# Kernel optimization log

Hardware: AMD Instinct MI355X
Metric: run time of the kernel (lower is better)

The kernel has to match this reference:

```python
import jax, jax.numpy as jnp
import numpy as np

N = 50000      # nodes
E = 800000     # edges
H = 128        # hidden_features
DEPTH = 5
G = 64         # graphs in batch
EPS = 1e-5


def _ln(x, g, b):
    m = jnp.mean(x, axis=-1, keepdims=True)
    v = jnp.mean((x - m) ** 2, axis=-1, keepdims=True)
    return (x - m) * jax.lax.rsqrt(v + EPS) * g + b


def _lin_init(key, fan_in, fan_out):
    s = 1.0 / np.sqrt(fan_in)
    kw, kb = jax.random.split(key)
    return (jax.random.uniform(kw, (fan_in, fan_out), jnp.float32, -s, s),
            jax.random.uniform(kb, (fan_out,), jnp.float32, -s, s))


def setup_inputs() -> dict:
    key = jax.random.key(0)
    ks = jax.random.split(key, 16)
    inp = {
        'x': jax.random.normal(ks[0], (N, 1), jnp.float32),
        'pos': jax.random.normal(ks[1], (N, 3), jnp.float32),
        'edge_index': jax.random.randint(ks[2], (2, E), 0, N, jnp.int32),
        'cell_offset': jax.random.normal(ks[3], (E, 3), jnp.float32),
        'unit_cell': jax.random.normal(ks[4], (3, 3), jnp.float32),
        'batch_ids': jnp.sort(jax.random.randint(ks[5], (N,), 0, G, jnp.int32)),
    }
    inp['emb_w'], inp['emb_b'] = _lin_init(ks[6], 1, H)
    # stacked per-layer params for lax.scan
    def stack(fn):
        outs = [fn(jax.random.fold_in(ks[7], i)) for i in range(DEPTH)]
        return tuple(jnp.stack(t) for t in zip(*outs))
    def layer_params(k):
        k1, k2, k3, k4 = jax.random.split(k, 4)
        mw1, mb1 = _lin_init(k1, 2 * H + 1, H)
        mw2, mb2 = _lin_init(k2, H, H)
        uw1, ub1 = _lin_init(k3, 2 * H, H)
        uw2, ub2 = _lin_init(k4, H, H)
        ones = jnp.ones((H,), jnp.float32); zeros = jnp.zeros((H,), jnp.float32)
        return (mw1, mb1, ones, zeros, mw2, mb2, ones, zeros,
                uw1, ub1, ones, zeros, uw2, ub2, ones, zeros)
    (inp['msg_w1'], inp['msg_b1'], inp['msg_g1'], inp['msg_be1'],
     inp['msg_w2'], inp['msg_b2'], inp['msg_g2'], inp['msg_be2'],
     inp['upd_w1'], inp['upd_b1'], inp['upd_g1'], inp['upd_be1'],
     inp['upd_w2'], inp['upd_b2'], inp['upd_g2'], inp['upd_be2']) = stack(layer_params)
    inp['pred_w1'], inp['pred_b1'] = _lin_init(ks[8], H, H)
    inp['pred_w2'], inp['pred_b2'] = _lin_init(ks[9], H, 1)
    return inp


def reference(x, pos, edge_index, cell_offset, unit_cell, batch_ids,
              emb_w, emb_b,
              msg_w1, msg_b1, msg_g1, msg_be1, msg_w2, msg_b2, msg_g2, msg_be2,
              upd_w1, upd_b1, upd_g1, upd_be1, upd_w2, upd_b2, upd_g2, upd_be2,
              pred_w1, pred_b1, pred_w2, pred_b2):
    src, dst = edge_index[0], edge_index[1]  # PyG: x_j = source, x_i = target
    h = x @ emb_w + emb_b  # [N, H]
    # PBC distances
    corrected = pos[dst] - cell_offset @ unit_cell  # [E, 3]
    dist = jnp.linalg.norm(corrected - pos[src], axis=-1, keepdims=True)  # [E, 1]

    def step(h, p):
        (mw1, mb1, mg1, mbe1, mw2, mb2, mg2, mbe2,
         uw1, ub1, ug1, ube1, uw2, ub2, ug2, ube2) = p
        msg = jnp.concatenate([h[dst], h[src], dist], axis=-1)  # [E, 2H+1]
        msg = jax.nn.relu(_ln(msg @ mw1 + mb1, mg1, mbe1))
        msg = jax.nn.relu(_ln(msg @ mw2 + mb2, mg2, mbe2))
        aggr = jax.ops.segment_sum(msg, dst, num_segments=N)  # scatter-add to targets
        u = jnp.concatenate([h, aggr], axis=-1)  # [N, 2H]
        u = jax.nn.relu(_ln(u @ uw1 + ub1, ug1, ube1))
        u = jax.nn.relu(_ln(u @ uw2 + ub2, ug2, ube2))
        return h + u, None  # residual

    params = (msg_w1, msg_b1, msg_g1, msg_be1, msg_w2, msg_b2, msg_g2, msg_be2,
              upd_w1, upd_b1, upd_g1, upd_be1, upd_w2, upd_b2, upd_g2, upd_be2)
    h, _ = jax.lax.scan(step, h, params)
    pooled = jax.ops.segment_sum(h, batch_ids, num_segments=G)  # global_add_pool
    return jax.nn.relu(pooled @ pred_w1 + pred_b1) @ pred_w2 + pred_b2  # [G, 1]
```

## Files before the change

kernel.cpp:

```cpp
#include <hip/hip_runtime.h>
#include <hip/hip_bf16.h>

#define NN 50000
#define NE 800000
#define HD 128
#define DEPTH 5
#define NG 64
#define LNEPS 1e-5f

typedef __attribute__((ext_vector_type(8))) short bf8;
typedef __attribute__((ext_vector_type(4))) float f4;

static __device__ __forceinline__ unsigned short bf1(float x) {
    __hip_bfloat16 b = __float2bfloat16(x);
    unsigned short r;
    __builtin_memcpy(&r, &b, 2);
    return r;
}
static __device__ __forceinline__ unsigned int cvt2(float a, float b) {
    float2 t; t.x = a; t.y = b;
    __hip_bfloat162 h = __float22bfloat162_rn(t);
    unsigned int r;
    __builtin_memcpy(&r, &h, 4);
    return r;
}


__global__ void pack_weights(const float* __restrict__ msg_w1, const float* __restrict__ msg_w2,
                             const float* __restrict__ upd_w1, const float* __restrict__ upd_w2,
                             unsigned short* __restrict__ packed) {
    const int which = blockIdx.y & 3, layer = blockIdx.y >> 2;
    const int t = blockIdx.x * 256 + threadIdx.x;
    unsigned short* lbase = packed + layer * 98304;
    if (which == 0) {
        if (t >= 32768) return;
        const int e = t & 7, l = (t >> 3) & 63, f = (t >> 9) & 15, s = t >> 13;
        const int kk = s*32 + ((l >> 4) << 3) + e;
        const int k = (kk & 7)*16 + (kk >> 3);
        const float* W = msg_w1 + layer*257*HD;
        const float v = (f < 8) ? W[k*HD + f*16 + (l & 15)]
                                : W[(k + 128)*HD + (f - 8)*16 + (l & 15)];
        lbase[t] = bf1(v);
        return;
    }
    const float* src; int K; unsigned short* dst;
    if (which == 1)      { src = msg_w2 + layer*HD*HD;  K = 128; dst = lbase + 32768; }
    else if (which == 2) { src = upd_w1 + layer*256*HD; K = 256; dst = lbase + 49152; }
    else                 { src = upd_w2 + layer*HD*HD;  K = 128; dst = lbase + 81920; }
    if (t >= K * HD) return;
    const int e = t & 7, l = (t >> 3) & 63, f = (t >> 9) & 7, s = t >> 12;
    const int kk = s*32 + ((l >> 4) << 3) + e;
    const int k = (which & 1) ? ((kk & 7)*16 + (kk >> 3)) : kk;
    const int n = f*16 + (l & 15);
    dst[t] = bf1(src[k*HD + n]);
}

__global__ void pack_sig(const float* __restrict__ msg_w1, const float* __restrict__ msg_g1,
                         const float* __restrict__ msg_be1, float* __restrict__ sig) {
    const int t = blockIdx.x * 256 + threadIdx.x;
    if (t >= DEPTH * 384) return;
    const int layer = t / 384, w3 = (t % 384) / 128, i = t % 128;
    const int col = (i & 7)*16 + (i >> 3);
    float v;
    if (w3 == 0)      v = msg_w1[layer*257*HD + 256*HD + col];
    else if (w3 == 1) v = msg_g1[layer*HD + col];
    else              v = msg_be1[layer*HD + col];
    sig[t] = v;
}

__global__ void pack_y0(const float* __restrict__ emb_w, const float* __restrict__ emb_b,
                        const float* __restrict__ msg_w1, const float* __restrict__ msg_b1,
                        float* __restrict__ y0ab) {
    const int t = threadIdx.x;
    const int half = t >> 7, c = t & 127;
    const float* W = msg_w1 + half*128*HD;
    float a = 0.f, b = 0.f;
    for (int k = 0; k < 128; ++k) {
        const float w = W[k*HD + c];
        a += emb_w[k] * w;
        b += emb_b[k] * w;
    }
    if (half == 0) b += msg_b1[c];
    const int i = half*128 + ((c & 15)*8 + (c >> 4));
    y0ab[i] = a; y0ab[256 + i] = b;
}

__global__ void embed_kernel(const float* __restrict__ x, const float* __restrict__ emb_w,
                             const float* __restrict__ emb_b, const float* __restrict__ y0ab,
                             float* __restrict__ h, unsigned short* __restrict__ hb,
                             unsigned short* __restrict__ y) {
    const int i = blockIdx.x * 256 + threadIdx.x;
    const int n = i >> 8, t = i & 255;
    const float xv = x[n];
    y[i] = bf1(xv * y0ab[t] + y0ab[256 + t]);
    if (t < 128) {
        const float v = xv * emb_w[t] + emb_b[t];
        h[n*HD + t] = v; hb[n*HD + t] = bf1(v);
    }
}

__global__ void hist_kernel(const int* __restrict__ ei, int* __restrict__ cnt) {
    const int e = blockIdx.x * 256 + threadIdx.x;
    atomicAdd(&cnt[ei[NE + e]], 1);
}

__global__ __launch_bounds__(1024) void scan_kernel(const int* __restrict__ cnt,
                                                    int* __restrict__ cur) {
    __shared__ int part[1024];
    const int t = threadIdx.x;
    const int per = 49;
    const int base = t * per;
    int s = 0;
    for (int i = 0; i < per; ++i) { const int idx = base + i; if (idx < NN) s += cnt[idx]; }
    part[t] = s; __syncthreads();
    for (int st = 1; st < 1024; st <<= 1) {
        const int v = (t >= st) ? part[t - st] : 0;
        __syncthreads();
        part[t] += v;
        __syncthreads();
    }
    int run = (t == 0) ? 0 : part[t - 1];
    for (int i = 0; i < per; ++i) {
        const int idx = base + i;
        if (idx < NN) { cur[idx] = run; run += cnt[idx]; }
    }
}

__global__ void scatter_kernel(const int* __restrict__ ei, int* __restrict__ cur,
                               int* __restrict__ sidx, int* __restrict__ ssrc,
                               int* __restrict__ sdst) {
    const int e = blockIdx.x * 256 + threadIdx.x;
    const int d = ei[NE + e];
    const int p = atomicAdd(&cur[d], 1);
    sidx[p] = e; ssrc[p] = ei[e]; sdst[p] = d;
}

__global__ void dist_kernel(const float* __restrict__ pos, const int* __restrict__ sidx,
                            const int* __restrict__ ssrc, const int* __restrict__ sdst,
                            const float* __restrict__ cell, const float* __restrict__ U,
                            float* __restrict__ dist) {
    const int p = blockIdx.x * 256 + threadIdx.x;
    const int e = sidx[p];
    const int s = ssrc[p], d = sdst[p];
    const float c0 = cell[e*3], c1 = cell[e*3+1], c2 = cell[e*3+2];
    const float ox = c0*U[0] + c1*U[3] + c2*U[6];
    const float oy = c0*U[1] + c1*U[4] + c2*U[7];
    const float oz = c0*U[2] + c1*U[5] + c2*U[8];
    const float dx = pos[d*3]   - ox - pos[s*3];
    const float dy = pos[d*3+1] - oy - pos[s*3+1];
    const float dz = pos[d*3+2] - oz - pos[s*3+2];
    dist[p] = sqrtf(dx*dx + dy*dy + dz*dz);
}

__global__ __launch_bounds__(128, 4) void edge_kernel(
    const unsigned short* __restrict__ y, const float* __restrict__ dist,
    const int* __restrict__ ssrc, const int* __restrict__ sdst,
    const unsigned short* __restrict__ pw2, const float* __restrict__ sig,
    const float* __restrict__ b2, const float* __restrict__ g2,
    const float* __restrict__ be2, float* __restrict__ aggr)
{
    __shared__ unsigned short lds[64 * 128];
    __shared__ int dstl[64];
    char* ldsb = (char*)lds;
    const int tid = threadIdx.x, blk = blockIdx.x;
    const int l = tid & 63, wv = tid >> 6;
    const int li = l & 15, gq = l >> 4;

    if (tid < 64) dstl[tid] = sdst[blk*64 + tid];

    {
        const int rl = l >> 1, half = l & 1;
        const int row = wv*32 + rl;
        const int e = blk*64 + row;
        const int dn = sdst[e], sn = ssrc[e];
        const float dv = dist[e];
        const unsigned short* pd = y + dn*256 + half*64;
        const unsigned short* pS = y + sn*256 + 128 + half*64;
        const float* wl = sig + half*64;

        float msum[64];
        #pragma unroll
        for (int c = 0; c < 8; ++c) {
            const uint4 ud = *(const uint4*)(pd + c*8);
            const uint4 us = *(const uint4*)(pS + c*8);
            const float4 wa = *(const float4*)(wl + c*8);
            const float4 wb = *(const float4*)(wl + c*8 + 4);
            const unsigned int du[4] = {ud.x, ud.y, ud.z, ud.w};
            const unsigned int su[4] = {us.x, us.y, us.z, us.w};
            const float ww[8] = {wa.x,wa.y,wa.z,wa.w, wb.x,wb.y,wb.z,wb.w};
            #pragma unroll
            for (int k = 0; k < 4; ++k) {
                const float d0 = __uint_as_float(du[k] << 16);
                const float d1 = __uint_as_float(du[k] & 0xffff0000u);
                const float s0 = __uint_as_float(su[k] << 16);
                const float s1 = __uint_as_float(su[k] & 0xffff0000u);
                msum[c*8 + 2*k]     = d0 + s0 + dv*ww[2*k];
                msum[c*8 + 2*k + 1] = d1 + s1 + dv*ww[2*k+1];
            }
        }
        float s1 = 0.f, s2 = 0.f;
        #pragma unroll
        for (int i = 0; i < 64; ++i) { s1 += msum[i]; s2 += msum[i]*msum[i]; }
        s1 += __shfl_xor(s1, 1);
        s2 += __shfl_xor(s2, 1);
        const float mean = s1 * (1.f/HD);
        const float rstd = rsqrtf(s2*(1.f/HD) - mean*mean + LNEPS);

        const float* g1p = sig + 128 + half*64;
        const float* e1p = sig + 256 + half*64;
        const int rsw = (row & 7) << 4;
        const int base = row*256 + half*128;
        #pragma unroll
        for (int c = 0; c < 8; ++c) {
            const float4 ga = *(const float4*)(g1p + c*8);
            const float4 gb = *(const float4*)(g1p + c*8 + 4);
            const float4 ea = *(const float4*)(e1p + c*8);
            const float4 eb = *(const float4*)(e1p + c*8 + 4);
            const float gg[8] = {ga.x,ga.y,ga.z,ga.w, gb.x,gb.y,gb.z,gb.w};
            const float ee[8] = {ea.x,ea.y,ea.z,ea.w, eb.x,eb.y,eb.z,eb.w};
            float t[8];
            #pragma unroll
            for (int k = 0; k < 8; ++k)
                t[k] = fmaxf((msum[c*8+k] - mean)*rstd*gg[k] + ee[k], 0.f);
            uint4 u;
            u.x = cvt2(t[0], t[1]); u.y = cvt2(t[2], t[3]);
            u.z = cvt2(t[4], t[5]); u.w = cvt2(t[6], t[7]);
            *(uint4*)(ldsb + ((base + c*16) ^ rsw)) = u;
        }
    }

    f4 acc2[2][8];
    #pragma unroll
    for (int m = 0; m < 2; ++m)
        #pragma unroll
        for (int f = 0; f < 8; ++f) { f4 z = {0.f,0.f,0.f,0.f}; acc2[m][f] = z; }
    #pragma unroll
    for (int s = 0; s < 4; ++s) {
        bf8 breg[8];
        #pragma unroll
        for (int f = 0; f < 8; ++f) breg[f] = *(const bf8*)(pw2 + s*4096 + f*512 + l*8);
        #pragma unroll
        for (int m = 0; m < 2; ++m) {
            const int ar = wv*32 + m*16 + li;
            const bf8 a = *(const bf8*)(ldsb + ((ar*256 + s*64 + gq*16) ^ ((ar & 7) << 4)));
            #pragma unroll
            for (int f = 0; f < 8; ++f)
                acc2[m][f] = __builtin_amdgcn_mfma_f32_16x16x32_bf16(a, breg[f], acc2[m][f], 0, 0, 0);
        }
    }

    {
        float bb2[8], gg2[8], be2v[8];
        #pragma unroll
        for (int f = 0; f < 8; ++f) {
            const int n = f*16 + li;
            bb2[f] = b2[n]; gg2[f] = g2[n]; be2v[f] = be2[n];
        }
        #pragma unroll
        for (int m = 0; m < 2; ++m) {
            float ps[4] = {0,0,0,0}, pq[4] = {0,0,0,0};
            #pragma unroll
            for (int f = 0; f < 8; ++f)
                #pragma unroll
                for (int r = 0; r < 4; ++r) {
                    const float v = acc2[m][f][r] + bb2[f];
                    acc2[m][f][r] = v;
                    ps[r] += v; pq[r] += v*v;
                }
            #pragma unroll
            for (int mm = 1; mm < 16; mm <<= 1)
                #pragma unroll
                for (int r = 0; r < 4; ++r) {
                    ps[r] += __shfl_xor(ps[r], mm);
                    pq[r] += __shfl_xor(pq[r], mm);
                }
            #pragma unroll
            for (int r = 0; r < 4; ++r) {
                const float mean = ps[r] * (1.f/HD);
                const float rstd = rsqrtf(pq[r]*(1.f/HD) - mean*mean + LNEPS);
                const int row = wv*32 + m*16 + gq*4 + r;
                float vv[8];
                #pragma unroll
                for (int f = 0; f < 8; ++f)
                    vv[f] = fmaxf((acc2[m][f][r] - mean)*rstd*gg2[f] + be2v[f], 0.f);
                uint4 u;
                u.x = cvt2(vv[0], vv[1]); u.y = cvt2(vv[2], vv[3]);
                u.z = cvt2(vv[4], vv[5]); u.w = cvt2(vv[6], vv[7]);
                *(uint4*)(ldsb + ((row*256 + li*16) ^ ((row & 7) << 4))) = u;
            }
        }
    }
    __syncthreads();

    {
        const int j = tid;
        const int jj = (j & 7)*16 + (j >> 3);
        int curd = dstl[0];
        float a0 = 0.f;
        #pragma unroll 4
        for (int row = 0; row < 64; ++row) {
            const int d = dstl[row];
            const unsigned short u = *(const unsigned short*)(ldsb + ((row*256 + j*2) ^ ((row & 7) << 4)));
            const float v = __uint_as_float(((unsigned int)u) << 16);
            if (d != curd) { unsafeAtomicAdd(&aggr[curd*HD + jj], a0); a0 = 0.f; curd = d; }
            a0 += v;
        }
        unsafeAtomicAdd(&aggr[curd*HD + jj], a0);
    }
}

__global__ __launch_bounds__(256, 4) void node_kernel(
    unsigned short* __restrict__ hb, float* __restrict__ aggr,
    const unsigned short* __restrict__ pw,
    const float* __restrict__ b1, const float* __restrict__ g1, const float* __restrict__ be1,
    const float* __restrict__ b2, const float* __restrict__ g2, const float* __restrict__ be2,
    float* __restrict__ h,
    const unsigned short* __restrict__ pwy, const float* __restrict__ b1y,
    unsigned short* __restrict__ y, int do_y)
{
    __shared__ unsigned short lds[64 * 128];
    char* ldsb = (char*)lds;
    const int tid = threadIdx.x, blk = blockIdx.x;
    const int l = tid & 63, wv = tid >> 6;
    const int li = l & 15, gq = l >> 4;

    const int row = wv*16 + li;
    const int nA = blk*64 + row;
    const int nc = (nA < NN) ? nA : NN - 1;
    const unsigned short* pH = hb + nc*HD + gq*8;
    float* pA = aggr + nc*HD + gq*8;

    f4 acc[8];
    #pragma unroll
    for (int f = 0; f < 8; ++f) { f4 z = {0.f,0.f,0.f,0.f}; acc[f] = z; }

    #pragma unroll
    for (int s = 0; s < 8; ++s) {
        bf8 breg[8];
        #pragma unroll
        for (int f = 0; f < 8; ++f) breg[f] = *(const bf8*)(pw + s*4096 + f*512 + l*8);
        bf8 a;
        if (s < 4) {
            a = *(const bf8*)(pH + s*32);
        } else {
            const float4 a0 = *(const float4*)(pA + (s-4)*32);
            const float4 a1 = *(const float4*)(pA + (s-4)*32 + 4);
            union { unsigned int u[4]; bf8 v; } pk;
            pk.u[0] = cvt2(a0.x, a0.y); pk.u[1] = cvt2(a0.z, a0.w);
            pk.u[2] = cvt2(a1.x, a1.y); pk.u[3] = cvt2(a1.z, a1.w);
            a = pk.v;
        }
        #pragma unroll
        for (int f = 0; f < 8; ++f)
            acc[f] = __builtin_amdgcn_mfma_f32_16x16x32_bf16(a, breg[f], acc[f], 0, 0, 0);
    }

    {
        const float4 z = {0.f,0.f,0.f,0.f};
        if (nA < NN) {
            #pragma unroll
            for (int s = 0; s < 4; ++s) { *(float4*)(pA + s*32) = z; *(float4*)(pA + s*32 + 4) = z; }
        }
    }

    {
        float bb[8], gg[8], be[8];
        #pragma unroll
        for (int f = 0; f < 8; ++f) {
            const int n = f*16 + li;
            bb[f] = b1[n]; gg[f] = g1[n]; be[f] = be1[n];
        }
        float ps[4] = {0,0,0,0}, pq[4] = {0,0,0,0};
        #pragma unroll
        for (int f = 0; f < 8; ++f)
            #pragma unroll
            for (int r = 0; r < 4; ++r) {
                const float v = acc[f][r] + bb[f];
                acc[f][r] = v;
                ps[r] += v; pq[r] += v*v;
            }
        #pragma unroll
        for (int mm = 1; mm < 16; mm <<= 1)
            #pragma unroll
            for (int r = 0; r < 4; ++r) {
                ps[r] += __shfl_xor(ps[r], mm);
                pq[r] += __shfl_xor(pq[r], mm);
            }
        #pragma unroll
        for (int r = 0; r < 4; ++r) {
            const float mean = ps[r] * (1.f/HD);
            const float rstd = rsqrtf(pq[r]*(1.f/HD) - mean*mean + LNEPS);
            const int rw = wv*16 + gq*4 + r;
            float vv[8];
            #pragma unroll
            for (int f = 0; f < 8; ++f)
                vv[f] = fmaxf((acc[f][r] - mean)*rstd*gg[f] + be[f], 0.f);
            uint4 u;
            u.x = cvt2(vv[0], vv[1]); u.y = cvt2(vv[2], vv[3]);
            u.z = cvt2(vv[4], vv[5]); u.w = cvt2(vv[6], vv[7]);
            *(uint4*)(ldsb + ((rw*256 + li*16) ^ ((rw & 15) << 4))) = u;
        }
    }

    const unsigned short* pw2 = pw + 32768;
    f4 acc2[8];
    #pragma unroll
    for (int f = 0; f < 8; ++f) { f4 z = {0.f,0.f,0.f,0.f}; acc2[f] = z; }
    #pragma unroll
    for (int s = 0; s < 4; ++s) {
        bf8 breg[8];
        #pragma unroll
        for (int f = 0; f < 8; ++f) breg[f] = *(const bf8*)(pw2 + s*4096 + f*512 + l*8);
        const int ar = wv*16 + li;
        const bf8 a = *(const bf8*)(ldsb + ((ar*256 + s*64 + gq*16) ^ ((ar & 15) << 4)));
        #pragma unroll
        for (int f = 0; f < 8; ++f)
            acc2[f] = __builtin_amdgcn_mfma_f32_16x16x32_bf16(a, breg[f], acc2[f], 0, 0, 0);
    }

    {
        float bb2[8], gg2[8], be2v[8];
        #pragma unroll
        for (int f = 0; f < 8; ++f) {
            const int n = f*16 + li;
            bb2[f] = b2[n]; gg2[f] = g2[n]; be2v[f] = be2[n];
        }
        float ps[4] = {0,0,0,0}, pq[4] = {0,0,0,0};
        #pragma unroll
        for (int f = 0; f < 8; ++f)
            #pragma unroll
            for (int r = 0; r < 4; ++r) {
                const float v = acc2[f][r] + bb2[f];
                acc2[f][r] = v;
                ps[r] += v; pq[r] += v*v;
            }
        #pragma unroll
        for (int mm = 1; mm < 16; mm <<= 1)
            #pragma unroll
            for (int r = 0; r < 4; ++r) {
                ps[r] += __shfl_xor(ps[r], mm);
                pq[r] += __shfl_xor(pq[r], mm);
            }
        #pragma unroll
        for (int r = 0; r < 4; ++r) {
            const int node = blk*64 + wv*16 + gq*4 + r;
            const float mean = ps[r] * (1.f/HD);
            const float rstd = rsqrtf(pq[r]*(1.f/HD) - mean*mean + LNEPS);
            const int rw = wv*16 + gq*4 + r;
            float nhv[8];
            if (node < NN) {
                #pragma unroll
                for (int f = 0; f < 8; ++f) {
                    const int n = f*16 + li;
                    float v = fmaxf((acc2[f][r] - mean)*rstd*gg2[f] + be2v[f], 0.f);
                    const int idx = node*HD + n;
                    const float nh = h[idx] + v;
                    h[idx] = nh; hb[idx] = bf1(nh);
                    nhv[f] = nh;
                }
            } else {
                #pragma unroll
                for (int f = 0; f < 8; ++f) nhv[f] = 0.f;
            }
            uint4 u;
            u.x = cvt2(nhv[0], nhv[1]); u.y = cvt2(nhv[2], nhv[3]);
            u.z = cvt2(nhv[4], nhv[5]); u.w = cvt2(nhv[6], nhv[7]);
            *(uint4*)(ldsb + ((rw*256 + li*16) ^ ((rw & 15) << 4))) = u;
        }
    }

    if (do_y) {
        f4 accy[16];
        #pragma unroll
        for (int f = 0; f < 16; ++f) { f4 z = {0.f,0.f,0.f,0.f}; accy[f] = z; }
        #pragma unroll
        for (int s = 0; s < 4; ++s) {
            const int ar = wv*16 + li;
            const bf8 a = *(const bf8*)(ldsb + ((ar*256 + s*64 + gq*16) ^ ((ar & 15) << 4)));
            #pragma unroll
            for (int fh = 0; fh < 2; ++fh) {
                bf8 breg[8];
                #pragma unroll
                for (int f = 0; f < 8; ++f)
                    breg[f] = *(const bf8*)(pwy + s*8192 + (fh*8 + f)*512 + l*8);
                #pragma unroll
                for (int f = 0; f < 8; ++f)
                    accy[fh*8 + f] = __builtin_amdgcn_mfma_f32_16x16x32_bf16(a, breg[f], accy[fh*8 + f], 0, 0, 0);
            }
        }
        float bv[8];
        #pragma unroll
        for (int f = 0; f < 8; ++f) bv[f] = b1y[f*16 + li];
        #pragma unroll
        for (int r = 0; r < 4; ++r) {
            const int node = blk*64 + wv*16 + gq*4 + r;
            if (node < NN) {
                uint4 u;
                u.x = cvt2(accy[0][r]+bv[0], accy[1][r]+bv[1]);
                u.y = cvt2(accy[2][r]+bv[2], accy[3][r]+bv[3]);
                u.z = cvt2(accy[4][r]+bv[4], accy[5][r]+bv[5]);
                u.w = cvt2(accy[6][r]+bv[6], accy[7][r]+bv[7]);
                *(uint4*)(y + node*256 + li*8) = u;
                uint4 v;
                v.x = cvt2(accy[8][r],  accy[9][r]);
                v.y = cvt2(accy[10][r], accy[11][r]);
                v.z = cvt2(accy[12][r], accy[13][r]);
                v.w = cvt2(accy[14][r], accy[15][r]);
                *(uint4*)(y + node*256 + 128 + li*8) = v;
            }
        }
    }
}

__global__ void pool_kernel(const float* __restrict__ h, const int* __restrict__ bids,
                            float* __restrict__ pooled) {
    const int j = threadIdx.x;
    const int n0 = blockIdx.x * 256;
    if (n0 >= NN) return;
    int cur = bids[n0];
    float acc = 0.f;
    for (int i = 0; i < 256; ++i) {
        const int n = n0 + i;
        if (n >= NN) break;
        const int b = bids[n];
        if (b != cur) { unsafeAtomicAdd(&pooled[cur*HD + j], acc); acc = 0.f; cur = b; }
        acc += h[n*HD + j];
    }
    unsafeAtomicAdd(&pooled[cur*HD + j], acc);
}

__global__ void pred_kernel(const float* __restrict__ pooled, const float* __restrict__ w1,
                            const float* __restrict__ pb1, const float* __restrict__ w2,
                            const float* __restrict__ pb2, float* __restrict__ out) {
    const int g = blockIdx.x, j = threadIdx.x;
    __shared__ float pg[128];
    __shared__ float red[128];
    pg[j] = pooled[g*HD + j];
    __syncthreads();
    float z = pb1[j];
    for (int k = 0; k < 128; ++k) z += pg[k] * w1[k*HD + j];
    red[j] = fmaxf(z, 0.f) * w2[j];
    __syncthreads();
    for (int st = 64; st > 0; st >>= 1) {
        if (j < st) red[j] += red[j + st];
        __syncthreads();
    }
    if (j == 0) out[g] = red[0] + pb2[0];
}

extern "C" void kernel_launch(void* const* d_in, const int* in_sizes, int n_in,
                              void* d_out, int out_size, void* d_ws, size_t ws_size,
                              hipStream_t stream) {
    const float* x       = (const float*)d_in[0];
    const float* pos     = (const float*)d_in[1];
    const int*   ei      = (const int*)  d_in[2];
    const float* cell    = (const float*)d_in[3];
    const float* U       = (const float*)d_in[4];
    const int*   bids    = (const int*)  d_in[5];
    const float* emb_w   = (const float*)d_in[6];
    const float* emb_b   = (const float*)d_in[7];
    const float* msg_w1  = (const float*)d_in[8];
    const float* msg_b1  = (const float*)d_in[9];
    const float* msg_g1  = (const float*)d_in[10];
    const float* msg_be1 = (const float*)d_in[11];
    const float* msg_w2  = (const float*)d_in[12];
    const float* msg_b2  = (const float*)d_in[13];
    const float* msg_g2  = (const float*)d_in[14];
    const float* msg_be2 = (const float*)d_in[15];
    const float* upd_w1  = (const float*)d_in[16];
    const float* upd_b1  = (const float*)d_in[17];
    const float* upd_g1  = (const float*)d_in[18];
    const float* upd_be1 = (const float*)d_in[19];
    const float* upd_w2  = (const float*)d_in[20];
    const float* upd_b2  = (const float*)d_in[21];
    const float* upd_g2  = (const float*)d_in[22];
    const float* upd_be2 = (const float*)d_in[23];
    const float* pred_w1 = (const float*)d_in[24];
    const float* pred_b1 = (const float*)d_in[25];
    const float* pred_w2 = (const float*)d_in[26];
    const float* pred_b2 = (const float*)d_in[27];

    char* ws = (char*)d_ws;
    float*          h      = (float*)          ws;
    unsigned short* hb     = (unsigned short*)(ws + 25600000);
    float*          aggr   = (float*)         (ws + 38400000);
    float*          dist   = (float*)         (ws + 64000000);
    float*          pooled = (float*)         (ws + 67200000);
    unsigned short* packed = (unsigned short*)(ws + 67232768);
    int*            cnt    = (int*)           (ws + 68215808);
    int*            cur    = (int*)           (ws + 68416512);
    int*            sidx   = (int*)           (ws + 68617216);
    int*            ssrc   = (int*)           (ws + 71817216);
    int*            sdst   = (int*)           (ws + 75017216);
    float*          sig    = (float*)         (ws + 78217216);
    float*          y0ab   = (float*)         (ws + 78224896);
    unsigned short* y      = (unsigned short*)(ws + 78226944);

    hipMemsetAsync(aggr, 0, (size_t)NN * HD * sizeof(float), stream);
    hipMemsetAsync(pooled, 0, (size_t)NG * HD * sizeof(float), stream);
    hipMemsetAsync(cnt, 0, (size_t)NN * sizeof(int), stream);

    dim3 pgrid(128, DEPTH * 4);
    pack_weights<<<pgrid, 256, 0, stream>>>(msg_w1, msg_w2, upd_w1, upd_w2, packed);
    pack_sig<<<(DEPTH*384 + 255)/256, 256, 0, stream>>>(msg_w1, msg_g1, msg_be1, sig);
    pack_y0<<<1, 256, 0, stream>>>(emb_w, emb_b, msg_w1, msg_b1, y0ab);
    embed_kernel<<<NN, 256, 0, stream>>>(x, emb_w, emb_b, y0ab, h, hb, y);

    hist_kernel<<<NE / 256, 256, 0, stream>>>(ei, cnt);
    scan_kernel<<<1, 1024, 0, stream>>>(cnt, cur);
    scatter_kernel<<<NE / 256, 256, 0, stream>>>(ei, cur, sidx, ssrc, sdst);
    dist_kernel<<<NE / 256, 256, 0, stream>>>(pos, sidx, ssrc, sdst, cell, U, dist);

    for (int layer = 0; layer < DEPTH; ++layer) {
        const unsigned short* pl = packed + layer * 98304;
        edge_kernel<<<NE / 64, 128, 0, stream>>>(
            y, dist, ssrc, sdst, pl + 32768, sig + layer*384,
            msg_b2 + layer*HD, msg_g2 + layer*HD, msg_be2 + layer*HD,
            aggr);
        const int do_y = (layer + 1 < DEPTH) ? 1 : 0;
        const int nl = do_y ? layer + 1 : layer;
        node_kernel<<<(NN + 63) / 64, 256, 0, stream>>>(
            hb, aggr, pl + 49152,
            upd_b1 + layer*HD, upd_g1 + layer*HD, upd_be1 + layer*HD,
            upd_b2 + layer*HD, upd_g2 + layer*HD, upd_be2 + layer*HD,
            h,
            packed + nl * 98304, msg_b1 + nl*HD, y, do_y);
    }

    pool_kernel<<<(NN + 255) / 256, 128, 0, stream>>>(h, bids, pooled);
    pred_kernel<<<NG, 128, 0, stream>>>(pooled, pred_w1, pred_b1, pred_w2, pred_b2, (float*)d_out);
}
```

Baseline: 1.336 ms.

## Split edge kernel work across four waves per 64-edge block

The edge kernel block grows from 128 to 256 threads, so each wave handles 16 edge rows instead of 32. Four lanes now share each row in the first-layer LayerNorm stage, with an extra shuffle step, and each wave issues one MFMA row-tile per k-step instead of two. The scatter-add phase splits the 64 rows into two halves, one per group of 128 threads. This cuts per-thread register use (32 msum values, 8 accumulators) and adds parallelism per block. In exchange, each wave must reload the B-weight registers for fewer rows, and segment boundaries at the half split cause extra atomics.

```diff
diff --git a/kernel.cpp b/kernel.cpp
--- a/kernel.cpp
+++ b/kernel.cpp
@@ -152,7 +152,7 @@
     dist[p] = sqrtf(dx*dx + dy*dy + dz*dz);
 }
 
-__global__ __launch_bounds__(128, 4) void edge_kernel(
+__global__ __launch_bounds__(256, 4) void edge_kernel(
     const unsigned short* __restrict__ y, const float* __restrict__ dist,
     const int* __restrict__ ssrc, const int* __restrict__ sdst,
     const unsigned short* __restrict__ pw2, const float* __restrict__ sig,
@@ -169,18 +169,18 @@
     if (tid < 64) dstl[tid] = sdst[blk*64 + tid];
 
     {
-        const int rl = l >> 1, half = l & 1;
-        const int row = wv*32 + rl;
+        const int rl = l >> 2, q = l & 3;
+        const int row = wv*16 + rl;
         const int e = blk*64 + row;
         const int dn = sdst[e], sn = ssrc[e];
         const float dv = dist[e];
-        const unsigned short* pd = y + dn*256 + half*64;
-        const unsigned short* pS = y + sn*256 + 128 + half*64;
-        const float* wl = sig + half*64;
-
-        float msum[64];
-        #pragma unroll
-        for (int c = 0; c < 8; ++c) {
+        const unsigned short* pd = y + dn*256 + q*32;
+        const unsigned short* pS = y + sn*256 + 128 + q*32;
+        const float* wl = sig + q*32;
+
+        float msum[32];
+        #pragma unroll
+        for (int c = 0; c < 4; ++c) {
             const uint4 ud = *(const uint4*)(pd + c*8);
             const uint4 us = *(const uint4*)(pS + c*8);
             const float4 wa = *(const float4*)(wl + c*8);
@@ -200,18 +200,18 @@
         }
         float s1 = 0.f, s2 = 0.f;
         #pragma unroll
-        for (int i = 0; i < 64; ++i) { s1 += msum[i]; s2 += msum[i]*msum[i]; }
-        s1 += __shfl_xor(s1, 1);
-        s2 += __shfl_xor(s2, 1);
+        for (int i = 0; i < 32; ++i) { s1 += msum[i]; s2 += msum[i]*msum[i]; }
+        s1 += __shfl_xor(s1, 1);  s2 += __shfl_xor(s2, 1);
+        s1 += __shfl_xor(s1, 2);  s2 += __shfl_xor(s2, 2);
         const float mean = s1 * (1.f/HD);
         const float rstd = rsqrtf(s2*(1.f/HD) - mean*mean + LNEPS);
 
-        const float* g1p = sig + 128 + half*64;
-        const float* e1p = sig + 256 + half*64;
+        const float* g1p = sig + 128 + q*32;
+        const float* e1p = sig + 256 + q*32;
         const int rsw = (row & 7) << 4;
-        const int base = row*256 + half*128;
-        #pragma unroll
-        for (int c = 0; c < 8; ++c) {
+        const int base = row*256 + q*64;
+        #pragma unroll
+        for (int c = 0; c < 4; ++c) {
             const float4 ga = *(const float4*)(g1p + c*8);
             const float4 gb = *(const float4*)(g1p + c*8 + 4);
             const float4 ea = *(const float4*)(e1p + c*8);
@@ -229,24 +229,19 @@
         }
     }
 
-    f4 acc2[2][8];
+    f4 acc2[8];
     #pragma unroll
-    for (int m = 0; m < 2; ++m)
-        #pragma unroll
-        for (int f = 0; f < 8; ++f) { f4 z = {0.f,0.f,0.f,0.f}; acc2[m][f] = z; }
+    for (int f = 0; f < 8; ++f) { f4 z = {0.f,0.f,0.f,0.f}; acc2[f] = z; }
     #pragma unroll
     for (int s = 0; s < 4; ++s) {
         bf8 breg[8];
         #pragma unroll
         for (int f = 0; f < 8; ++f) breg[f] = *(const bf8*)(pw2 + s*4096 + f*512 + l*8);
-        #pragma unroll
-        for (int m = 0; m < 2; ++m) {
-            const int ar = wv*32 + m*16 + li;
-            const bf8 a = *(const bf8*)(ldsb + ((ar*256 + s*64 + gq*16) ^ ((ar & 7) << 4)));
-            #pragma unroll
-            for (int f = 0; f < 8; ++f)
-                acc2[m][f] = __builtin_amdgcn_mfma_f32_16x16x32_bf16(a, breg[f], acc2[m][f], 0, 0, 0);
-        }
+        const int ar = wv*16 + li;
+        const bf8 a = *(const bf8*)(ldsb + ((ar*256 + s*64 + gq*16) ^ ((ar & 7) << 4)));
+        #pragma unroll
+        for (int f = 0; f < 8; ++f)
+            acc2[f] = __builtin_amdgcn_mfma_f32_16x16x32_bf16(a, breg[f], acc2[f], 0, 0, 0);
     }
 
     {
@@ -256,49 +251,48 @@
             const int n = f*16 + li;
             bb2[f] = b2[n]; gg2[f] = g2[n]; be2v[f] = be2[n];
         }
-        #pragma unroll
-        for (int m = 0; m < 2; ++m) {
-            float ps[4] = {0,0,0,0}, pq[4] = {0,0,0,0};
+        float ps[4] = {0,0,0,0}, pq[4] = {0,0,0,0};
+        #pragma unroll
+        for (int f = 0; f < 8; ++f)
+            #pragma unroll
+            for (int r = 0; r < 4; ++r) {
+                const float v = acc2[f][r] + bb2[f];
+                acc2[f][r] = v;
+                ps[r] += v; pq[r] += v*v;
+            }
+        #pragma unroll
+        for (int mm = 1; mm < 16; mm <<= 1)
+            #pragma unroll
+            for (int r = 0; r < 4; ++r) {
+                ps[r] += __shfl_xor(ps[r], mm);
+                pq[r] += __shfl_xor(pq[r], mm);
+            }
+        #pragma unroll
+        for (int r = 0; r < 4; ++r) {
+            const float mean = ps[r] * (1.f/HD);
+            const float rstd = rsqrtf(pq[r]*(1.f/HD) - mean*mean + LNEPS);
+            const int row = wv*16 + gq*4 + r;
+            float vv[8];
             #pragma unroll
             for (int f = 0; f < 8; ++f)
-                #pragma unroll
-                for (int r = 0; r < 4; ++r) {
-                    const float v = acc2[m][f][r] + bb2[f];
-                    acc2[m][f][r] = v;
-                    ps[r] += v; pq[r] += v*v;
-                }
-            #pragma unroll
-            for (int mm = 1; mm < 16; mm <<= 1)
-                #pragma unroll
-                for (int r = 0; r < 4; ++r) {
-                    ps[r] += __shfl_xor(ps[r], mm);
-                    pq[r] += __shfl_xor(pq[r], mm);
-                }
-            #pragma unroll
-            for (int r = 0; r < 4; ++r) {
-                const float mean = ps[r] * (1.f/HD);
-                const float rstd = rsqrtf(pq[r]*(1.f/HD) - mean*mean + LNEPS);
-                const int row = wv*32 + m*16 + gq*4 + r;
-                float vv[8];
-                #pragma unroll
-                for (int f = 0; f < 8; ++f)
-                    vv[f] = fmaxf((acc2[m][f][r] - mean)*rstd*gg2[f] + be2v[f], 0.f);
-                uint4 u;
-                u.x = cvt2(vv[0], vv[1]); u.y = cvt2(vv[2], vv[3]);
-                u.z = cvt2(vv[4], vv[5]); u.w = cvt2(vv[6], vv[7]);
-                *(uint4*)(ldsb + ((row*256 + li*16) ^ ((row & 7) << 4))) = u;
-            }
+                vv[f] = fmaxf((acc2[f][r] - mean)*rstd*gg2[f] + be2v[f], 0.f);
+            uint4 u;
+            u.x = cvt2(vv[0], vv[1]); u.y = cvt2(vv[2], vv[3]);
+            u.z = cvt2(vv[4], vv[5]); u.w = cvt2(vv[6], vv[7]);
+            *(uint4*)(ldsb + ((row*256 + li*16) ^ ((row & 7) << 4))) = u;
         }
     }
     __syncthreads();
 
     {
-        const int j = tid;
+        const int j = tid & 127, hh = tid >> 7;
         const int jj = (j & 7)*16 + (j >> 3);
-        int curd = dstl[0];
+        const int r0 = hh * 32;
+        int curd = dstl[r0];
         float a0 = 0.f;
         #pragma unroll 4
-        for (int row = 0; row < 64; ++row) {
+        for (int i = 0; i < 32; ++i) {
+            const int row = r0 + i;
             const int d = dstl[row];
             const unsigned short u = *(const unsigned short*)(ldsb + ((row*256 + j*2) ^ ((row & 7) << 4)));
             const float v = __uint_as_float(((unsigned int)u) << 16);
@@ -613,7 +607,7 @@
 
     for (int layer = 0; layer < DEPTH; ++layer) {
         const unsigned short* pl = packed + layer * 98304;
-        edge_kernel<<<NE / 64, 128, 0, stream>>>(
+        edge_kernel<<<NE / 64, 256, 0, stream>>>(
             y, dist, ssrc, sdst, pl + 32768, sig + layer*384,
             msg_b2 + layer*HD, msg_g2 + layer*HD, msg_be2 + layer*HD,
             aggr);
```

Result: slower. 1.731 ms (+29.5%).
